# Kernel optimization log

Measured on AMD Instinct MI355X. Metric: run time of the kernel, lower is better.

The kernel has to match this reference:

```python
import jax, jax.numpy as jnp
import numpy as np
from jax import lax

EPOCHS = 3
N_IN, N_OUT = 20, 18
BN_EPS = 1e-5
RECT_EPS = 1e-4
TRIU = np.triu_indices(N_OUT)  # SPDVectorize upper-triangular indices


def _orth(key, n, m):
    # Stiefel init: orthonormal columns, like nn.init.orthogonal_
    q, _ = jnp.linalg.qr(jax.random.normal(key, (n, m), dtype=jnp.float32))
    return q


def setup_inputs() -> dict:
    key = jax.random.key(0)
    ks = jax.random.split(key, 8)
    bs = 2048
    f32 = jnp.float32
    return dict(
        x=jax.random.normal(ks[0], (bs, 1, 22, 438), dtype=f32),
        W1=jax.random.normal(ks[1], (22, 1, 22, 1), dtype=f32) * 0.1,
        b1=jnp.zeros((22,), f32),
        g1=jnp.ones((22,), f32), be1=jnp.zeros((22,), f32),
        W2=jax.random.normal(ks[2], (20, 22, 1, 12), dtype=f32) * 0.05,
        b2=jnp.zeros((20,), f32),
        g2=jnp.ones((20,), f32), be2=jnp.zeros((20,), f32),
        Wq=_orth(ks[3], N_IN, N_OUT),
        Wk=_orth(ks[4], N_IN, N_OUT),
        Wv=_orth(ks[5], N_IN, N_OUT),
        Wl=jax.random.normal(ks[6], (N_OUT * (N_OUT + 1) // 2 * EPOCHS, 4), dtype=f32) * 0.02,
        bl=jnp.zeros((4,), f32),
    )


def _bn(x, g, b):
    # BatchNorm2d forward in training mode (batch statistics, biased var)
    mean = x.mean(axis=(0, 2, 3), keepdims=True)
    var = ((x - mean) ** 2).mean(axis=(0, 2, 3), keepdims=True)
    return (x - mean) * lax.rsqrt(var + BN_EPS) * g[None, :, None, None] + b[None, :, None, None]


def _conv(x, w, b, pad_w):
    y = lax.conv_general_dilated(x, w, (1, 1), [(0, 0), (pad_w, pad_w)],
                                 dimension_numbers=('NCHW', 'OIHW', 'NCHW'))
    return y + b[None, :, None, None]


def _signal2spd(x):
    # x: (bs, C, L) -> trace-normalized covariance + 1e-5 * I
    L = x.shape[-1]
    xc = x - x.mean(-1, keepdims=True)
    cov = jnp.einsum('bcl,bdl->bcd', xc, xc) / (L - 1)
    cov = cov / jnp.trace(cov, axis1=-2, axis2=-1)[:, None, None]
    return cov + 1e-5 * jnp.eye(cov.shape[-1], dtype=cov.dtype)


def _patch_lens(n, epochs):
    base = n // epochs
    lens = [base] * epochs
    for i in range(n - base * epochs):
        lens[i] += 1
    return lens


def _spd_fn(t, fn):
    # SPD functional calculus via eigh (== torch.svd on SPD input)
    s, u = jnp.linalg.eigh(t)
    return jnp.einsum('...ij,...j,...kj->...ik', u, fn(s), u)


def _forward(x, W1, b1, g1, be1, W2, b2, g2, be2, Wq, Wk, Wv, Wl, bl):
    bs = x.shape[0]
    h = _bn(_conv(x, W1, b1, 0), g1, be1)          # (bs,22,1,438)
    h = _bn(_conv(h, W2, b2, 6), g2, be2)          # (bs,20,1,439)
    sig = h[:, :, 0, :]                            # squeeze -> (bs,20,439)
    covs, off = [], 0
    for L in _patch_lens(sig.shape[-1], EPOCHS):   # E2R: [147,146,146]
        covs.append(_signal2spd(sig[:, :, off:off + L]))
        off += L
    X = jnp.stack(covs, axis=1)                    # (bs,m,20,20) SPD
    # SPDTransform: W^T X W with Stiefel W (20,18)
    Q = jnp.einsum('pi,bmpq,qj->bmij', Wq, X, Wq)
    K = jnp.einsum('pi,bmpq,qj->bmij', Wk, X, Wk)
    V = jnp.einsum('pi,bmpq,qj->bmij', Wv, X, Wv)
    logQ = _spd_fn(Q, jnp.log)
    logK = _spd_fn(K, jnp.log)
    logV = _spd_fn(V, jnp.log)
    # log-Euclidean distance^2: ||log Q_j - log K_i||_F^2  (== sum of svd singvals of D D^T)
    diff = logQ[:, :, None] - logK[:, None, :]     # (bs, mq, mk, n, n)
    energy = jnp.sum(diff * diff, axis=(-2, -1))   # (bs, mq, mk)
    scores = 1.0 / (1.0 + jnp.log1p(energy))
    # torch: softmax over dim=-2 then permute(0,2,1) == softmax over K index here
    P = jax.nn.softmax(scores, axis=-1)            # (bs, mq, mk)
    mixed = jnp.einsum('bji,bipq->bjpq', P, logV)  # weighted log-Euclidean mean
    out = _spd_fn(mixed, jnp.exp)
    out = _spd_fn(out, lambda s: jnp.maximum(s, RECT_EPS))  # SPDRectified
    logO = _spd_fn(out, jnp.log)                   # SPDTangentSpace log
    vec = logO[..., TRIU[0], TRIU[1]]              # (bs, m, 171)
    return vec.reshape(bs, -1) @ Wl + bl           # (bs, 4)


def reference(x, W1, b1, g1, be1, W2, b2, g2, be2, Wq, Wk, Wv, Wl, bl):
    return _forward(x, W1, b1, g1, be1, W2, b2, g2, be2, Wq, Wk, Wv, Wl, bl)
```

## Files before the change

### kernel.cpp

```cpp
#include <hip/hip_runtime.h>
#include <math.h>

#define OFF_Y2   0
#define OFF_QKV  17981440
#define OFF_ST   (17981440 + 5971968)
#define ST_SX   0
#define ST_SXX  22
#define ST_WF   506
#define ST_BF   990
#define ST_Y2S  1012
#define ST_Y2Q  1032
#define ST_TOT  1052

#define LOGEPS -9.210340371976182f
#define NSWEEP 5
#define SHIFT  12.0f

__global__ __launch_bounds__(256) void k0_zero(float* __restrict__ st){
  for (int i = threadIdx.x; i < ST_TOT; i += 256) st[i] = 0.f;
}

__global__ __launch_bounds__(256) void k1_xstats(const float* __restrict__ x, float* __restrict__ st){
  __shared__ __align__(16) float xs[22*444];
  const float* xb = x + (size_t)blockIdx.x * (22*438);
  for (int i = threadIdx.x; i < 22*444; i += 256){
    int h = i / 444, w = i - h*444;
    xs[i] = (w < 438) ? xb[h*438 + w] : 0.f;
  }
  __syncthreads();
  for (int t = threadIdx.x; t < 275; t += 256){
    if (t < 22){
      const float4* r = (const float4*)&xs[t*444];
      float4 acc = {0.f,0.f,0.f,0.f};
      for (int w = 0; w < 111; ++w){ float4 v = r[w]; acc.x+=v.x; acc.y+=v.y; acc.z+=v.z; acc.w+=v.w; }
      atomicAdd(&st[ST_SX + t], acc.x+acc.y+acc.z+acc.w);
    } else {
      int rem = t - 22, h = 0;
      while (rem >= 22 - h){ rem -= 22 - h; ++h; }
      int h2 = h + rem;
      const float4* ra = (const float4*)&xs[h*444];
      const float4* rb = (const float4*)&xs[h2*444];
      float4 acc = {0.f,0.f,0.f,0.f};
      for (int w = 0; w < 111; ++w){
        float4 a = ra[w], b = rb[w];
        acc.x = fmaf(a.x,b.x,acc.x); acc.y = fmaf(a.y,b.y,acc.y);
        acc.z = fmaf(a.z,b.z,acc.z); acc.w = fmaf(a.w,b.w,acc.w);
      }
      atomicAdd(&st[ST_SXX + h*22 + h2], acc.x+acc.y+acc.z+acc.w);
    }
  }
}

__global__ __launch_bounds__(64) void k1b_fold(const float* __restrict__ W1, const float* __restrict__ g1,
                                               const float* __restrict__ be1, float* __restrict__ st){
  int c = threadIdx.x;
  if (c >= 22) return;
  const float invN = 1.f / (2048.f*438.f);
  float mcol[22];
  float mu0 = 0.f;
  for (int h = 0; h < 22; ++h){ mcol[h] = W1[c*22 + h]; mu0 = fmaf(mcol[h], st[ST_SX + h], mu0); }
  mu0 *= invN;
  float qf = 0.f;
  for (int h = 0; h < 22; ++h)
    for (int h2 = h; h2 < 22; ++h2){
      float w = mcol[h]*mcol[h2]*st[ST_SXX + h*22 + h2];
      qf += (h2 == h) ? w : 2.f*w;
    }
  qf *= invN;
  float var = qf - mu0*mu0;
  float a1 = g1[c] * rsqrtf(var + 1e-5f);
  for (int h = 0; h < 22; ++h) st[ST_WF + h*22 + c] = a1 * mcol[h];
  st[ST_BF + c] = be1[c] - a1 * mu0;
}

__global__ __launch_bounds__(256) void k2_weff(const float* __restrict__ W2, const float* __restrict__ st,
                                               float* __restrict__ weff, float* __restrict__ pfx){
  __shared__ float wf[484];
  __shared__ float bf[22];
  for (int i = threadIdx.x; i < 484; i += 256) wf[i] = st[ST_WF + i];
  if (threadIdx.x < 22) bf[threadIdx.x] = st[ST_BF + threadIdx.x];
  __syncthreads();
  for (int i = threadIdx.x; i < 5280; i += 256){
    int d = i / 264, r = i - d*264, h = r / 12, t = r - h*12;
    float a = 0.f;
    for (int c = 0; c < 22; ++c) a = fmaf(W2[d*264 + c*12 + t], wf[h*22 + c], a);
    weff[i] = a;
  }
  if (threadIdx.x < 20){
    int d = threadIdx.x;
    float run = 0.f;
    pfx[d*13 + 0] = 0.f;
    for (int t = 0; t < 12; ++t){
      float a = 0.f;
      for (int c = 0; c < 22; ++c) a = fmaf(W2[d*264 + c*12 + t], bf[c], a);
      run += a;
      pfx[d*13 + t + 1] = run;
    }
  }
}

__global__ __launch_bounds__(256, 5) void k3_conv(const float* __restrict__ x,
    const float* __restrict__ weff, const float* __restrict__ pfx,
    float* __restrict__ st, float* __restrict__ y2){
  __shared__ __align__(16) float xs[22*236];
  __shared__ __align__(16) float ws[10*264];
  __shared__ float ps[130];
  __shared__ float sloc[10], qloc[10];
  int tid = threadIdx.x;
  int dh = blockIdx.x & 1, wh = blockIdx.x >> 1;
  int n = blockIdx.y;
  int wbase = wh*220, dbase = dh*10;
  const float* xb = x + (size_t)n*9636;
  for (int i = tid; i < 22*232; i += 256){
    int h = i / 232, lw = i - h*232;
    int gw = wbase - 6 + lw;
    xs[h*236 + lw] = (gw >= 0 && gw < 438) ? xb[h*438 + gw] : 0.f;
  }
  for (int i = tid; i < 2640; i += 256) ws[i] = weff[dbase*264 + i];
  if (tid < 130) ps[tid] = pfx[dbase*13 + tid];
  if (tid < 10){ sloc[tid] = 0.f; qloc[tid] = 0.f; }
  __syncthreads();
  if (tid < 220){
    int dl = tid / 22, wc = tid - dl*22;
    float acc[10];
    #pragma unroll
    for (int j = 0; j < 10; ++j) acc[j] = 0.f;
    #pragma unroll 1
    for (int h = 0; h < 22; ++h){
      const float* xr = &xs[h*236 + wc*10];
      float xw[21];
      #pragma unroll
      for (int k = 0; k < 10; ++k) *(float2*)&xw[2*k] = *(const float2*)&xr[2*k];
      xw[20] = xr[20];
      const float* wr = &ws[dl*264 + h*12];
      float wt[12];
      #pragma unroll
      for (int t = 0; t < 12; t += 4){ float4 v = *(const float4*)&wr[t]; wt[t]=v.x; wt[t+1]=v.y; wt[t+2]=v.z; wt[t+3]=v.w; }
      #pragma unroll
      for (int t = 0; t < 12; ++t)
        #pragma unroll
        for (int j = 0; j < 10; ++j)
          acc[j] = fmaf(wt[t], xw[j+t], acc[j]);
    }
    int d = dbase + dl;
    float* yb = y2 + (size_t)n*8780 + d*439;
    const float* pr = &ps[dl*13];
    float s = 0.f, q = 0.f;
    int w0 = wbase + wc*10;
    #pragma unroll
    for (int j = 0; j < 10; ++j){
      int gw = w0 + j;
      if (gw < 439){
        int lo = 6 - gw; lo = (lo > 0) ? lo : 0;
        int hi = 444 - gw; hi = (hi < 12) ? hi : 12;
        float val = acc[j] + pr[hi] - pr[lo];
        yb[gw] = val;
        s += val; q = fmaf(val, val, q);
      }
    }
    atomicAdd(&sloc[dl], s);
    atomicAdd(&qloc[dl], q);
  }
  __syncthreads();
  if (tid < 10){
    atomicAdd(&st[ST_Y2S + dbase + tid], sloc[tid]);
    atomicAdd(&st[ST_Y2Q + dbase + tid], qloc[tid]);
  }
}

__global__ __launch_bounds__(256) void k4_cov_qkv(const float* __restrict__ y2, const float* __restrict__ st,
    const float* __restrict__ g2, const float* __restrict__ Wq, const float* __restrict__ Wk,
    const float* __restrict__ Wv, float* __restrict__ qkv){
  __shared__ __align__(16) float ysp[3][20][148];
  __shared__ float a2s[20];
  __shared__ __align__(16) float Bt[3][18][20];
  __shared__ __align__(16) float G3[3][400];
  __shared__ __align__(16) float Tmt[3][360];
  __shared__ float musum3[3][20];
  __shared__ float rtr3[3];
  int tid = threadIdx.x, n = blockIdx.x;
  if (tid < 20){
    const float invN = 1.f/(2048.f*439.f);
    float s = st[ST_Y2S + tid]*invN;
    float q = st[ST_Y2Q + tid]*invN;
    a2s[tid] = g2[tid] * rsqrtf(q - s*s + 1e-5f);
  }
  const float* yb = y2 + (size_t)n*8780;
  for (int i = tid; i < 8780; i += 256){
    int d = i/439, w = i - d*439;
    int m = (w >= 293) ? 2 : ((w >= 147) ? 1 : 0);
    int lw = w - ((m == 2) ? 293 : ((m == 1) ? 147 : 0));
    ysp[m][d][lw] = yb[i];
  }
  if (tid < 100){
    int d = tid/5, k = tid - d*5;
    int m = (k == 0) ? 0 : ((k < 3) ? 1 : 2);
    int lw = (k == 0) ? 147 : ((k == 1 || k == 3) ? 146 : 147);
    ysp[m][d][lw] = 0.f;
  }
  __syncthreads();
  for (int i = tid; i < 1140; i += 256){
    if (i < 1080){
      int wt = i/360, r = i - wt*360; int d = r/18, jj = r - d*18;
      const float* Wm = (wt==0) ? Wq : ((wt==1) ? Wk : Wv);
      Bt[wt][jj][d] = a2s[d]*Wm[d*18 + jj];
    } else {
      int t = i - 1080; int m = t/20, d = t - m*20;
      const float4* r = (const float4*)&ysp[m][d][0];
      float4 acc = {0.f,0.f,0.f,0.f};
      #pragma unroll 1
      for (int w = 0; w < 37; ++w){ float4 v = r[w]; acc.x+=v.x; acc.y+=v.y; acc.z+=v.z; acc.w+=v.w; }
      musum3[m][d] = acc.x+acc.y+acc.z+acc.w;
    }
  }
  __syncthreads();
  for (int it = tid; it < 630; it += 256){
    int m = it/210, t = it - m*210;
    int rem = t, c = 0;
    while (rem >= 20 - c){ rem -= 20 - c; ++c; }
    int d = c + rem;
    const float4* ra = (const float4*)&ysp[m][c][0];
    const float4* rb = (const float4*)&ysp[m][d][0];
    float4 acc4 = {0.f,0.f,0.f,0.f};
    #pragma unroll 1
    for (int w = 0; w < 37; ++w){
      float4 a = ra[w], b = rb[w];
      acc4.x = fmaf(a.x,b.x,acc4.x); acc4.y = fmaf(a.y,b.y,acc4.y);
      acc4.z = fmaf(a.z,b.z,acc4.z); acc4.w = fmaf(a.w,b.w,acc4.w);
    }
    float invL = (m == 0) ? (1.f/147.f) : (1.f/146.f);
    float acc = (acc4.x+acc4.y+acc4.z+acc4.w) - musum3[m][c]*musum3[m][d]*invL;
    G3[m][c*20 + d] = acc; G3[m][d*20 + c] = acc;
  }
  __syncthreads();
  for (int wt = 0; wt < 3; ++wt){
    for (int i = tid; i < 1083; i += 256){
      if (i < 1080){
        int m = i/360, r = i - m*360; int p = r/18, jj = r - p*18;
        const float4* gr = (const float4*)&G3[m][p*20];
        const float4* br = (const float4*)&Bt[wt][jj][0];
        float4 a4 = {0.f,0.f,0.f,0.f};
        #pragma unroll
        for (int w = 0; w < 5; ++w){
          float4 a = gr[w], b = br[w];
          a4.x = fmaf(a.x,b.x,a4.x); a4.y = fmaf(a.y,b.y,a4.y);
          a4.z = fmaf(a.z,b.z,a4.z); a4.w = fmaf(a.w,b.w,a4.w);
        }
        Tmt[m][jj*20 + p] = a4.x+a4.y+a4.z+a4.w;
      } else if (wt == 0){
        int m = i - 1080;
        float tr = 0.f;
        for (int c = 0; c < 20; ++c){ float a = a2s[c]; tr = fmaf(a*a, G3[m][c*21], tr); }
        rtr3[m] = 1.f/tr;
      }
    }
    __syncthreads();
    for (int it = tid; it < 513; it += 256){
      int m = it/171, t = it - m*171;
      int rem = t, i = 0;
      while (rem >= 18 - i){ rem -= 18 - i; ++i; }
      int jj = i + rem;
      const float4* br = (const float4*)&Bt[wt][i][0];
      const float4* tr = (const float4*)&Tmt[m][jj*20];
      float4 a4 = {0.f,0.f,0.f,0.f};
      #pragma unroll
      for (int w = 0; w < 5; ++w){
        float4 a = br[w], b = tr[w];
        a4.x = fmaf(a.x,b.x,a4.x); a4.y = fmaf(a.y,b.y,a4.y);
        a4.z = fmaf(a.z,b.z,a4.z); a4.w = fmaf(a.w,b.w,a4.w);
      }
      float acc = (a4.x+a4.y+a4.z+a4.w) * rtr3[m];
      if (i == jj) acc += 1e-5f;
      float* outm = qkv + ((size_t)wt*6144 + (size_t)n*3 + m)*324;
      outm[i*18 + jj] = acc; outm[jj*18 + i] = acc;
    }
    __syncthreads();
  }
}

__global__ __launch_bounds__(256, 4) void k5_oneside(const float* __restrict__ src, float* __restrict__ dst,
    int nmat, int mode, const float* __restrict__ Wl, const float* __restrict__ bl,
    float* __restrict__ outp){
  __shared__ __align__(16) float stage[12][384];
  __shared__ __align__(16) float wls[2052];
  __shared__ float outacc[4][4];
  int tid = threadIdx.x;
  int wave = tid >> 6, lane = tid & 63;
  int g = (lane >= 54) ? 3 : (lane >= 36 ? 2 : (lane >= 18 ? 1 : 0));
  int j = lane - g*18;
  int gb = g*18;
  int slot = wave*3 + ((g < 3) ? g : 0);
  int mat = blockIdx.x*12 + wave*3 + g;
  bool act = (g < 3) && (mat < nmat);

  if (mode == 1){
    for (int i = tid; i < 2052; i += 256) wls[i] = Wl[i];
    if (tid < 16) outacc[tid >> 2][tid & 3] = 0.f;
  }

  float b[18];
  float sh = (mode == 1) ? SHIFT : 0.f;
  if (act){
    const float* s = src + (size_t)mat*324 + j*18;
    #pragma unroll
    for (int i = 0; i < 18; ++i) b[i] = s[i] + ((i == j) ? sh : 0.f);
  } else {
    #pragma unroll
    for (int i = 0; i < 18; ++i) b[i] = (i == j) ? 1.f : 0.f;
  }
  float nrm;
  { float n0 = 0.f, n1 = 0.f;
    #pragma unroll
    for (int k = 0; k < 18; k += 2){ n0 = fmaf(b[k],b[k],n0); n1 = fmaf(b[k+1],b[k+1],n1); }
    nrm = n0 + n1; }

  #pragma unroll 1
  for (int sweep = 0; sweep < NSWEEP; ++sweep){
    #pragma unroll
    for (int r = 0; r < 17; ++r){
      int xx = j - 1 - r; if (xx < 0) xx += 17;
      int v = r + 17 - xx; if (v >= 17) v -= 17;
      int m = (j == 0) ? (1 + r) : ((xx == 0) ? 0 : (1 + v));
      bool isp = (j == 0) ? true : ((xx == 0) ? false : (xx <= 8));
      int plane = (gb + m) & 63;
      float rv[18];
      #pragma unroll
      for (int k = 0; k < 18; ++k) rv[k] = __shfl(b[k], plane);
      float on = __shfl(nrm, plane);
      float g0 = 0.f, g1 = 0.f;
      #pragma unroll
      for (int k = 0; k < 18; k += 2){ g0 = fmaf(b[k], rv[k], g0); g1 = fmaf(b[k+1], rv[k+1], g1); }
      float gam = g0 + g1;
      float alpha = isp ? nrm : on;
      float beta  = isp ? on  : nrm;
      float tau = (beta - alpha) * 0.5f * __builtin_amdgcn_rcpf(gam);
      float tt = __builtin_amdgcn_rcpf(fabsf(tau) + sqrtf(fmaf(tau, tau, 1.f)));
      float t = (tau >= 0.f) ? tt : -tt;
      if (!(fabsf(gam) > 1e-36f)) t = 0.f;
      float c = __builtin_amdgcn_rsqf(fmaf(t, t, 1.f));
      float s = t*c;
      nrm = fmaf(isp ? -t : t, gam, nrm);
      float sg = isp ? -s : s;
      #pragma unroll
      for (int k = 0; k < 18; ++k) b[k] = fmaf(c, b[k], sg*rv[k]);
    }
  }
  float n0 = 0.f, n1 = 0.f;
  #pragma unroll
  for (int k = 0; k < 18; k += 2){ n0 = fmaf(b[k],b[k],n0); n1 = fmaf(b[k+1],b[k+1],n1); }
  float nf = fmaxf(n0 + n1, 1e-30f);
  float fv = (mode == 0) ? (0.5f * logf(nf)) : fmaxf(sqrtf(nf) - SHIFT, LOGEPS);
  float wv = fv * __builtin_amdgcn_rcpf(nf);
  float* sp = &stage[slot][0];
  if (act){
    #pragma unroll
    for (int k = 0; k < 18; ++k) sp[k*20 + j] = b[k];
    sp[360 + j] = wv;
  }
  __syncthreads();
  if (act){
    float wr[18];
    #pragma unroll
    for (int i = 0; i < 18; ++i) wr[i] = sp[j*20 + i] * sp[360 + i];
    float frow[18];
    #pragma unroll
    for (int i2 = 0; i2 < 18; ++i2){
      const float* br = &sp[i2*20];
      float a0 = 0.f;
      #pragma unroll
      for (int k = 0; k < 16; k += 4){
        float4 v4 = *(const float4*)&br[k];
        a0 = fmaf(wr[k],   v4.x, a0); a0 = fmaf(wr[k+1], v4.y, a0);
        a0 = fmaf(wr[k+2], v4.z, a0); a0 = fmaf(wr[k+3], v4.w, a0);
      }
      a0 = fmaf(wr[16], br[16], a0);
      a0 = fmaf(wr[17], br[17], a0);
      frow[i2] = a0;
    }
    if (mode == 0){
      float* orow = dst + (size_t)mat*324 + j*18;
      #pragma unroll
      for (int i2 = 0; i2 < 18; ++i2) orow[i2] = frow[i2];
    } else {
      int base = (g*171 + j*(37 - j)/2 - j)*4;
      float o0=0.f, o1=0.f, o2=0.f, o3=0.f;
      #pragma unroll
      for (int jj = 0; jj < 18; ++jj){
        if (jj >= j){
          const float* w4 = &wls[base + jj*4];
          o0 = fmaf(frow[jj], w4[0], o0);
          o1 = fmaf(frow[jj], w4[1], o1);
          o2 = fmaf(frow[jj], w4[2], o2);
          o3 = fmaf(frow[jj], w4[3], o3);
        }
      }
      atomicAdd(&outacc[wave][0], o0);
      atomicAdd(&outacc[wave][1], o1);
      atomicAdd(&outacc[wave][2], o2);
      atomicAdd(&outacc[wave][3], o3);
    }
  }
  if (mode == 1){
    __syncthreads();
    if (tid < 16){
      int bi = tid >> 2, o = tid & 3;
      outp[(blockIdx.x*4 + bi)*4 + o] = outacc[bi][o] + bl[o];
    }
  }
}

__global__ __launch_bounds__(128) void k6_attnmix(const float* __restrict__ logs, float* __restrict__ mixed){
  __shared__ float lq[972], lk[972], lv[972];
  __shared__ float ew[2][9];
  __shared__ float P[9];
  int b = blockIdx.x, tid = threadIdx.x;
  const float* q  = logs + (size_t)b*972;
  const float* k_ = logs + 1990656 + (size_t)b*972;
  const float* v_ = logs + 3981312 + (size_t)b*972;
  for (int i = tid; i < 972; i += 128){ lq[i] = q[i]; lk[i] = k_[i]; lv[i] = v_[i]; }
  __syncthreads();
  float e[9] = {0.f,0.f,0.f,0.f,0.f,0.f,0.f,0.f,0.f};
  for (int x = tid; x < 324; x += 128){
    float q0 = lq[x], q1 = lq[324+x], q2 = lq[648+x];
    float k0 = lk[x], k1 = lk[324+x], k2 = lk[648+x];
    float d;
    d = q0-k0; e[0] = fmaf(d,d,e[0]);
    d = q0-k1; e[1] = fmaf(d,d,e[1]);
    d = q0-k2; e[2] = fmaf(d,d,e[2]);
    d = q1-k0; e[3] = fmaf(d,d,e[3]);
    d = q1-k1; e[4] = fmaf(d,d,e[4]);
    d = q1-k2; e[5] = fmaf(d,d,e[5]);
    d = q2-k0; e[6] = fmaf(d,d,e[6]);
    d = q2-k1; e[7] = fmaf(d,d,e[7]);
    d = q2-k2; e[8] = fmaf(d,d,e[8]);
  }
  #pragma unroll
  for (int p = 0; p < 9; ++p)
    for (int off = 32; off; off >>= 1) e[p] += __shfl_down(e[p], off);
  if ((tid & 63) == 0){
    #pragma unroll
    for (int p = 0; p < 9; ++p) ew[tid >> 6][p] = e[p];
  }
  __syncthreads();
  if (tid < 3){
    float en0 = ew[0][tid*3+0] + ew[1][tid*3+0];
    float en1 = ew[0][tid*3+1] + ew[1][tid*3+1];
    float en2 = ew[0][tid*3+2] + ew[1][tid*3+2];
    float s0 = 1.f/(1.f + log1pf(en0));
    float s1 = 1.f/(1.f + log1pf(en1));
    float s2 = 1.f/(1.f + log1pf(en2));
    float mx = fmaxf(s0, fmaxf(s1, s2));
    float e0 = expf(s0-mx), e1 = expf(s1-mx), e2 = expf(s2-mx);
    float inv = 1.f/(e0+e1+e2);
    P[tid*3+0] = e0*inv; P[tid*3+1] = e1*inv; P[tid*3+2] = e2*inv;
  }
  __syncthreads();
  float p00=P[0],p01=P[1],p02=P[2],p10=P[3],p11=P[4],p12=P[5],p20=P[6],p21=P[7],p22=P[8];
  float* mb = mixed + (size_t)b*972;
  for (int x = tid; x < 324; x += 128){
    float v0 = lv[x], v1 = lv[324+x], v2 = lv[648+x];
    mb[x]     = p00*v0 + p01*v1 + p02*v2;
    mb[324+x] = p10*v0 + p11*v1 + p12*v2;
    mb[648+x] = p20*v0 + p21*v1 + p22*v2;
  }
}

extern "C" void kernel_launch(void* const* d_in, const int* in_sizes, int n_in,
                              void* d_out, int out_size, void* d_ws, size_t ws_size,
                              hipStream_t stream){
  (void)in_sizes; (void)n_in; (void)out_size; (void)ws_size;
  const float* x   = (const float*)d_in[0];
  const float* W1  = (const float*)d_in[1];
  const float* g1  = (const float*)d_in[3];
  const float* be1 = (const float*)d_in[4];
  const float* W2  = (const float*)d_in[5];
  const float* g2  = (const float*)d_in[7];
  const float* Wq  = (const float*)d_in[9];
  const float* Wk  = (const float*)d_in[10];
  const float* Wv  = (const float*)d_in[11];
  const float* Wl  = (const float*)d_in[12];
  const float* bl  = (const float*)d_in[13];
  float* ws    = (float*)d_ws;
  float* y2    = ws + OFF_Y2;
  float* qkv   = ws + OFF_QKV;
  float* weff  = ws + OFF_QKV;
  float* pfx   = ws + OFF_QKV + 5280;
  float* logs  = ws + OFF_Y2;
  float* mixed = ws + OFF_QKV;
  float* st    = ws + OFF_ST;
  float* outp  = (float*)d_out;

  k0_zero    <<<dim3(1),       dim3(256), 0, stream>>>(st);
  k1_xstats  <<<dim3(2048),    dim3(256), 0, stream>>>(x, st);
  k1b_fold   <<<dim3(1),       dim3(64),  0, stream>>>(W1, g1, be1, st);
  k2_weff    <<<dim3(1),       dim3(256), 0, stream>>>(W2, st, weff, pfx);
  k3_conv    <<<dim3(4,2048),  dim3(256), 0, stream>>>(x, weff, pfx, st, y2);
  k4_cov_qkv <<<dim3(2048),    dim3(256), 0, stream>>>(y2, st, g2, Wq, Wk, Wv, qkv);
  k5_oneside <<<dim3(1536),    dim3(256), 0, stream>>>(qkv, logs, 18432, 0, nullptr, nullptr, nullptr);
  k6_attnmix <<<dim3(2048),    dim3(128), 0, stream>>>(logs, mixed);
  k5_oneside <<<dim3(512),     dim3(256), 0, stream>>>(mixed, nullptr, 6144, 1, Wl, bl, outp);
}
```

Baseline: 788.8 us.

## Restructure conv kernel to one output channel per wave with scalar weights

```diff
diff --git a/kernel.cpp b/kernel.cpp
--- a/kernel.cpp
+++ b/kernel.cpp
@@ -99,72 +99,71 @@
   }
 }
 
-__global__ __launch_bounds__(256, 5) void k3_conv(const float* __restrict__ x,
+__global__ __launch_bounds__(256, 8) void k3_conv(const float* __restrict__ x,
     const float* __restrict__ weff, const float* __restrict__ pfx,
     float* __restrict__ st, float* __restrict__ y2){
-  __shared__ __align__(16) float xs[22*236];
-  __shared__ __align__(16) float ws[10*264];
-  __shared__ float ps[130];
-  __shared__ float sloc[10], qloc[10];
+  __shared__ __align__(16) float xs[22*232];
   int tid = threadIdx.x;
-  int dh = blockIdx.x & 1, wh = blockIdx.x >> 1;
+  int wave = tid >> 6, lane = tid & 63;
+  int wh = blockIdx.x & 1, dq = blockIdx.x >> 1;
   int n = blockIdx.y;
-  int wbase = wh*220, dbase = dh*10;
+  int d = dq*4 + wave;
+  int wbase = wh*220;
   const float* xb = x + (size_t)n*9636;
   for (int i = tid; i < 22*232; i += 256){
     int h = i / 232, lw = i - h*232;
     int gw = wbase - 6 + lw;
-    xs[h*236 + lw] = (gw >= 0 && gw < 438) ? xb[h*438 + gw] : 0.f;
-  }
-  for (int i = tid; i < 2640; i += 256) ws[i] = weff[dbase*264 + i];
-  if (tid < 130) ps[tid] = pfx[dbase*13 + tid];
-  if (tid < 10){ sloc[tid] = 0.f; qloc[tid] = 0.f; }
-  __syncthreads();
-  if (tid < 220){
-    int dl = tid / 22, wc = tid - dl*22;
-    float acc[10];
-    #pragma unroll
-    for (int j = 0; j < 10; ++j) acc[j] = 0.f;
-    #pragma unroll 1
-    for (int h = 0; h < 22; ++h){
-      const float* xr = &xs[h*236 + wc*10];
-      float xw[21];
-      #pragma unroll
-      for (int k = 0; k < 10; ++k) *(float2*)&xw[2*k] = *(const float2*)&xr[2*k];
-      xw[20] = xr[20];
-      const float* wr = &ws[dl*264 + h*12];
-      float wt[12];
-      #pragma unroll
-      for (int t = 0; t < 12; t += 4){ float4 v = *(const float4*)&wr[t]; wt[t]=v.x; wt[t+1]=v.y; wt[t+2]=v.z; wt[t+3]=v.w; }
-      #pragma unroll
-      for (int t = 0; t < 12; ++t)
-        #pragma unroll
-        for (int j = 0; j < 10; ++j)
-          acc[j] = fmaf(wt[t], xw[j+t], acc[j]);
-    }
-    int d = dbase + dl;
-    float* yb = y2 + (size_t)n*8780 + d*439;
-    const float* pr = &ps[dl*13];
-    float s = 0.f, q = 0.f;
-    int w0 = wbase + wc*10;
-    #pragma unroll
-    for (int j = 0; j < 10; ++j){
-      int gw = w0 + j;
+    xs[i] = (gw >= 0 && gw < 438) ? xb[h*438 + gw] : 0.f;
+  }
+  __syncthreads();
+  int dsc = __builtin_amdgcn_readfirstlane(d);
+  const float* wp = weff + dsc*264;
+  bool act = lane < 44;
+  int base = act ? lane*5 : 0;
+  float acc[5] = {0.f,0.f,0.f,0.f,0.f};
+  #pragma unroll 1
+  for (int h = 0; h < 22; ++h){
+    float4 w0 = *(const float4*)(wp + h*12);
+    float4 w1 = *(const float4*)(wp + h*12 + 4);
+    float4 w2 = *(const float4*)(wp + h*12 + 8);
+    float wt[12] = {w0.x,w0.y,w0.z,w0.w, w1.x,w1.y,w1.z,w1.w, w2.x,w2.y,w2.z,w2.w};
+    const float* xr = &xs[h*232 + base];
+    float xw[16];
+    #pragma unroll
+    for (int k = 0; k < 16; ++k) xw[k] = xr[k];
+    #pragma unroll
+    for (int t = 0; t < 12; ++t)
+      #pragma unroll
+      for (int j = 0; j < 5; ++j)
+        acc[j] = fmaf(wt[t], xw[j+t], acc[j]);
+  }
+  float s = 0.f, q = 0.f;
+  if (act){
+    const float* prd = pfx + dsc*13;
+    float bias12 = prd[12];
+    float* yb = y2 + (size_t)n*8780 + (size_t)d*439;
+    #pragma unroll
+    for (int j = 0; j < 5; ++j){
+      int gw = wbase + base + j;
       if (gw < 439){
-        int lo = 6 - gw; lo = (lo > 0) ? lo : 0;
-        int hi = 444 - gw; hi = (hi < 12) ? hi : 12;
-        float val = acc[j] + pr[hi] - pr[lo];
+        float bias;
+        if (gw >= 6 && gw <= 432) bias = bias12;
+        else {
+          int lo = 6 - gw; if (lo < 0) lo = 0;
+          int hi = 444 - gw; if (hi > 12) hi = 12;
+          bias = prd[hi] - prd[lo];
+        }
+        float val = acc[j] + bias;
         yb[gw] = val;
         s += val; q = fmaf(val, val, q);
       }
     }
-    atomicAdd(&sloc[dl], s);
-    atomicAdd(&qloc[dl], q);
-  }
-  __syncthreads();
-  if (tid < 10){
-    atomicAdd(&st[ST_Y2S + dbase + tid], sloc[tid]);
-    atomicAdd(&st[ST_Y2Q + dbase + tid], qloc[tid]);
+  }
+  #pragma unroll
+  for (int off = 32; off; off >>= 1){ s += __shfl_down(s, off); q += __shfl_down(q, off); }
+  if (lane == 0){
+    atomicAdd(&st[ST_Y2S + d], s);
+    atomicAdd(&st[ST_Y2Q + d], q);
   }
 }
 
@@ -494,7 +493,7 @@
   k1_xstats  <<<dim3(2048),    dim3(256), 0, stream>>>(x, st);
   k1b_fold   <<<dim3(1),       dim3(64),  0, stream>>>(W1, g1, be1, st);
   k2_weff    <<<dim3(1),       dim3(256), 0, stream>>>(W2, st, weff, pfx);
-  k3_conv    <<<dim3(4,2048),  dim3(256), 0, stream>>>(x, weff, pfx, st, y2);
+  k3_conv    <<<dim3(10,2048), dim3(256), 0, stream>>>(x, weff, pfx, st, y2);
   k4_cov_qkv <<<dim3(2048),    dim3(256), 0, stream>>>(y2, st, g2, Wq, Wk, Wv, qkv);
   k5_oneside <<<dim3(1536),    dim3(256), 0, stream>>>(qkv, logs, 18432, 0, nullptr, nullptr, nullptr);
   k6_attnmix <<<dim3(2048),    dim3(128), 0, stream>>>(logs, mixed);
```

After: 1.428 ms. +81.1%, slower.
